# Kernel optimization log

Measured on AMD Instinct MI355X. Metric: run time of the kernel, lower is better.

Reference implementation:

```python
import jax, jax.numpy as jnp
import numpy as np


def _blur(x1, kernel):
    # x1: [B,H,W,1], kernel: [k,k,1,1]; 'same' padding conv, stride 1
    return jax.lax.conv_general_dilated(
        x1, kernel, window_strides=(1, 1), padding='SAME',
        dimension_numbers=('NHWC', 'HWIO', 'NHWC'))


def setup_inputs() -> dict:
    key = jax.random.key(0)
    kx, kk = jax.random.split(key)
    B, H, W, C = 32, 512, 512, 3
    KSZ = 9
    x = jax.random.normal(kx, (B, H, W, C), dtype=jnp.float32)
    # Gaussian-random kernel ~ N(1, 0.05), normalized to sum to 1 (as in normal_kernel)
    kernel = 1.0 + 0.05 * jax.random.normal(kk, (KSZ, KSZ, 1, 1), dtype=jnp.float32)
    kernel = kernel / jnp.sum(kernel)
    return {'x': x, 'kernel': kernel}


def reference(x, kernel):
    # conv2d helper in the original convolves each channel with the SAME kernel
    # then averages across channels; that equals convolving the channel-mean once.
    local_mean = _blur(jnp.mean(x, axis=-1, keepdims=True), kernel)   # [B,H,W,1]
    v = x - local_mean                                                # [B,H,W,C]
    sigma = jnp.sqrt(_blur(jnp.mean(jnp.square(v), axis=-1, keepdims=True), kernel))  # [B,H,W,1]
    mean_sigma = jnp.mean(sigma, axis=(1, 2), keepdims=True)          # [B,1,1,1]
    return v / jnp.maximum(mean_sigma, sigma)
```

## Files before the change

### kernel.cpp

```cpp
#include <hip/hip_runtime.h>

#define BB 32
#define HH 512
#define WW 512
#define HW (HH * WW)
#define NPIX (BB * HH * WW)

#define TILE 64
#define HALO 4
#define RG 72
#define RQ 18
#define NQ (RG * RQ)

__global__ __launch_bounds__(256) void k_moments(const float4* __restrict__ x4,
                                                 float4* __restrict__ m4,
                                                 float4* __restrict__ q4,
                                                 float* __restrict__ sums) {
    int g = blockIdx.x * 256 + threadIdx.x;
    if (blockIdx.x == 0 && threadIdx.x < BB) sums[threadIdx.x] = 0.f;
    if (g >= NPIX / 4) return;
    float4 a = x4[3 * g + 0];
    float4 b = x4[3 * g + 1];
    float4 c = x4[3 * g + 2];
    const float t = 1.f / 3.f;
    float4 m, q;
    m.x = (a.x + a.y + a.z) * t;  q.x = (a.x * a.x + a.y * a.y + a.z * a.z) * t;
    m.y = (a.w + b.x + b.y) * t;  q.y = (a.w * a.w + b.x * b.x + b.y * b.y) * t;
    m.z = (b.z + b.w + c.x) * t;  q.z = (b.z * b.z + b.w * b.w + c.x * c.x) * t;
    m.w = (c.y + c.z + c.w) * t;  q.w = (c.y * c.y + c.z * c.z + c.w * c.w) * t;
    m4[g] = m;
    q4[g] = q;
}

__global__ __launch_bounds__(256) void k_blur_m(const float* __restrict__ src,
                                                const float* __restrict__ kw,
                                                float* __restrict__ dst) {
    __shared__ float tile[RG * RG];
    __shared__ float kk[81];
    const int tx = threadIdx.x, ty = threadIdx.y;
    const int tid = ty * 16 + tx;
    if (tid < 81) kk[tid] = kw[tid];
    const int x0 = blockIdx.x * TILE, y0 = blockIdx.y * TILE;
    const float4* s4 = (const float4*)(src + (size_t)blockIdx.z * HW);
    for (int i = tid; i < NQ; i += 256) {
        int r = i / RQ, q = i - r * RQ;
        int gy = y0 + r - HALO, gx = x0 + 4 * q - HALO;
        float4 v = make_float4(0.f, 0.f, 0.f, 0.f);
        if (gy >= 0 && gy < HH && gx >= 0 && gx < WW) v = s4[(gy * WW + gx) >> 2];
        *(float4*)&tile[r * RG + 4 * q] = v;
    }
    __syncthreads();

    float acc[4][4] = {};
    const float4* t4 = (const float4*)tile;
#pragma unroll
    for (int ky = 0; ky < 9; ++ky) {
        float w[9];
#pragma unroll
        for (int kx = 0; kx < 9; ++kx) w[kx] = kk[ky * 9 + kx];
#pragma unroll
        for (int my = 0; my < 4; ++my) {
            int rr = (4 * ty + my + ky) * RQ + tx;
            float4 a = t4[rr], b = t4[rr + 1], c = t4[rr + 2];
            float f[12] = {a.x, a.y, a.z, a.w, b.x, b.y, b.z, b.w, c.x, c.y, c.z, c.w};
#pragma unroll
            for (int kx = 0; kx < 9; ++kx)
#pragma unroll
                for (int mx = 0; mx < 4; ++mx)
                    acc[my][mx] = fmaf(w[kx], f[mx + kx], acc[my][mx]);
        }
    }
    float* dp = dst + (size_t)blockIdx.z * HW + (size_t)(y0 + 4 * ty) * WW + x0 + 4 * tx;
#pragma unroll
    for (int my = 0; my < 4; ++my)
        *(float4*)(dp + my * WW) = make_float4(acc[my][0], acc[my][1], acc[my][2], acc[my][3]);
}

__global__ __launch_bounds__(256) void k_sigma(const float* __restrict__ m,
                                               const float* __restrict__ q,
                                               const float* __restrict__ lm,
                                               const float* __restrict__ kw,
                                               float* __restrict__ sg,
                                               float* __restrict__ sums) {
    __shared__ float tile[RG * RG];
    __shared__ float kk[81];
    __shared__ float wsum[4];
    const int tx = threadIdx.x, ty = threadIdx.y;
    const int tid = ty * 16 + tx;
    if (tid < 81) kk[tid] = kw[tid];
    const int x0 = blockIdx.x * TILE, y0 = blockIdx.y * TILE;
    const size_t boff = (size_t)blockIdx.z * HW;
    const float4* m4 = (const float4*)(m + boff);
    const float4* q4 = (const float4*)(q + boff);
    const float4* l4 = (const float4*)(lm + boff);
    for (int i = tid; i < NQ; i += 256) {
        int r = i / RQ, qd = i - r * RQ;
        int gy = y0 + r - HALO, gx = x0 + 4 * qd - HALO;
        float4 e = make_float4(0.f, 0.f, 0.f, 0.f);
        if (gy >= 0 && gy < HH && gx >= 0 && gx < WW) {
            int o = (gy * WW + gx) >> 2;
            float4 mm = m4[o], qq = q4[o], ll = l4[o];
            e.x = fmaxf(qq.x - ll.x * (2.f * mm.x - ll.x), 0.f);
            e.y = fmaxf(qq.y - ll.y * (2.f * mm.y - ll.y), 0.f);
            e.z = fmaxf(qq.z - ll.z * (2.f * mm.z - ll.z), 0.f);
            e.w = fmaxf(qq.w - ll.w * (2.f * mm.w - ll.w), 0.f);
        }
        *(float4*)&tile[r * RG + 4 * qd] = e;
    }
    __syncthreads();

    float acc[4][4] = {};
    const float4* t4 = (const float4*)tile;
#pragma unroll
    for (int ky = 0; ky < 9; ++ky) {
        float w[9];
#pragma unroll
        for (int kx = 0; kx < 9; ++kx) w[kx] = kk[ky * 9 + kx];
#pragma unroll
        for (int my = 0; my < 4; ++my) {
            int rr = (4 * ty + my + ky) * RQ + tx;
            float4 a = t4[rr], b = t4[rr + 1], c = t4[rr + 2];
            float f[12] = {a.x, a.y, a.z, a.w, b.x, b.y, b.z, b.w, c.x, c.y, c.z, c.w};
#pragma unroll
            for (int kx = 0; kx < 9; ++kx)
#pragma unroll
                for (int mx = 0; mx < 4; ++mx)
                    acc[my][mx] = fmaf(w[kx], f[mx + kx], acc[my][mx]);
        }
    }
    float s = 0.f;
    float* dp = sg + boff + (size_t)(y0 + 4 * ty) * WW + x0 + 4 * tx;
#pragma unroll
    for (int my = 0; my < 4; ++my) {
        float4 o;
        o.x = sqrtf(fmaxf(acc[my][0], 0.f));
        o.y = sqrtf(fmaxf(acc[my][1], 0.f));
        o.z = sqrtf(fmaxf(acc[my][2], 0.f));
        o.w = sqrtf(fmaxf(acc[my][3], 0.f));
        *(float4*)(dp + my * WW) = o;
        s += o.x + o.y + o.z + o.w;
    }
#pragma unroll
    for (int off = 32; off > 0; off >>= 1) s += __shfl_down(s, off);
    if ((tid & 63) == 0) wsum[tid >> 6] = s;
    __syncthreads();
    if (tid == 0) atomicAdd(&sums[blockIdx.z], wsum[0] + wsum[1] + wsum[2] + wsum[3]);
}

__global__ __launch_bounds__(256) void k_norm(const float4* __restrict__ x4,
                                              const float4* __restrict__ lm4,
                                              const float4* __restrict__ sg4,
                                              const float* __restrict__ sums,
                                              float4* __restrict__ out4) {
    int g = blockIdx.x * 256 + threadIdx.x;
    if (g >= NPIX / 4) return;
    int b = (g * 4) / HW;
    float ms = sums[b] * (1.f / (float)HW);
    float4 l = lm4[g];
    float4 s = sg4[g];
    float i0 = 1.f / fmaxf(ms, s.x);
    float i1 = 1.f / fmaxf(ms, s.y);
    float i2 = 1.f / fmaxf(ms, s.z);
    float i3 = 1.f / fmaxf(ms, s.w);
    float4 a = x4[3 * g + 0];
    float4 bb = x4[3 * g + 1];
    float4 c = x4[3 * g + 2];
    float4 o0, o1, o2;
    o0.x = (a.x - l.x) * i0;  o0.y = (a.y - l.x) * i0;  o0.z = (a.z - l.x) * i0;
    o0.w = (a.w - l.y) * i1;  o1.x = (bb.x - l.y) * i1; o1.y = (bb.y - l.y) * i1;
    o1.z = (bb.z - l.z) * i2; o1.w = (bb.w - l.z) * i2; o2.x = (c.x - l.z) * i2;
    o2.y = (c.y - l.w) * i3;  o2.z = (c.z - l.w) * i3;  o2.w = (c.w - l.w) * i3;
    out4[3 * g + 0] = o0;
    out4[3 * g + 1] = o1;
    out4[3 * g + 2] = o2;
}

extern "C" void kernel_launch(void* const* d_in, const int* in_sizes, int n_in,
                              void* d_out, int out_size, void* d_ws, size_t ws_size,
                              hipStream_t stream) {
    const float* x = (const float*)d_in[0];
    const float* kw = (const float*)d_in[1];
    float* out = (float*)d_out;
    float* wsp = (float*)d_ws;
    float* m    = wsp + 0 * (size_t)NPIX;
    float* q    = wsp + 1 * (size_t)NPIX;
    float* lm   = wsp + 2 * (size_t)NPIX;
    float* sg   = wsp + 3 * (size_t)NPIX;
    float* sums = wsp + 4 * (size_t)NPIX;

    const int ngrp = NPIX / 4;
    k_moments<<<ngrp / 256, 256, 0, stream>>>((const float4*)x, (float4*)m, (float4*)q, sums);

    dim3 blk(16, 16);
    dim3 grd(WW / TILE, HH / TILE, BB);
    k_blur_m<<<grd, blk, 0, stream>>>(m, kw, lm);
    k_sigma<<<grd, blk, 0, stream>>>(m, q, lm, kw, sg, sums);

    k_norm<<<ngrp / 256, 256, 0, stream>>>((const float4*)x, (const float4*)lm,
                                           (const float4*)sg, sums, (float4*)out);
}
```

Measured before the change: 299.1 us.

## Fuse moments, mean blur and sigma blur into one tiled kernel

Merges the channel-moment pass, the local-mean blur and the sigma blur into a single kernel. Each 64x64 tile loads x with an 8-pixel halo, computes mean and square moments in shared memory, and blurs the mean over the 72x72 inner region (recomputing halo work). It then forms the per-pixel variance term in place and blurs it again. This removes the global round trips for m, q and lm between kernels. Per-batch sums are now written as per-block partials and reduced in k_norm, replacing the atomics and the zeroing step. The costs are redundant halo compute, larger shared memory use that may lower occupancy, and filter weights read directly from global memory.

```diff
diff --git a/kernel.cpp b/kernel.cpp
--- a/kernel.cpp
+++ b/kernel.cpp
@@ -7,161 +7,168 @@
 #define NPIX (BB * HH * WW)
 
 #define TILE 64
-#define HALO 4
-#define RG 72
-#define RQ 18
-#define NQ (RG * RQ)
-
-__global__ __launch_bounds__(256) void k_moments(const float4* __restrict__ x4,
-                                                 float4* __restrict__ m4,
-                                                 float4* __restrict__ q4,
-                                                 float* __restrict__ sums) {
-    int g = blockIdx.x * 256 + threadIdx.x;
-    if (blockIdx.x == 0 && threadIdx.x < BB) sums[threadIdx.x] = 0.f;
-    if (g >= NPIX / 4) return;
-    float4 a = x4[3 * g + 0];
-    float4 b = x4[3 * g + 1];
-    float4 c = x4[3 * g + 2];
-    const float t = 1.f / 3.f;
-    float4 m, q;
-    m.x = (a.x + a.y + a.z) * t;  q.x = (a.x * a.x + a.y * a.y + a.z * a.z) * t;
-    m.y = (a.w + b.x + b.y) * t;  q.y = (a.w * a.w + b.x * b.x + b.y * b.y) * t;
-    m.z = (b.z + b.w + c.x) * t;  q.z = (b.z * b.z + b.w * b.w + c.x * c.x) * t;
-    m.w = (c.y + c.z + c.w) * t;  q.w = (c.y * c.y + c.z * c.z + c.w * c.w) * t;
-    m4[g] = m;
-    q4[g] = q;
-}
-
-__global__ __launch_bounds__(256) void k_blur_m(const float* __restrict__ src,
-                                                const float* __restrict__ kw,
-                                                float* __restrict__ dst) {
-    __shared__ float tile[RG * RG];
-    __shared__ float kk[81];
+#define H2 8
+#define RG2 80
+#define RQ2 21
+#define RS2 84
+
+#define LOADROW12(dst, p4, base)                                              \
+    {                                                                         \
+        float4 A_ = (p4)[base], B_ = (p4)[(base) + 1], C_ = (p4)[(base) + 2]; \
+        (dst)[0] = A_.x; (dst)[1] = A_.y; (dst)[2]  = A_.z; (dst)[3]  = A_.w; \
+        (dst)[4] = B_.x; (dst)[5] = B_.y; (dst)[6]  = B_.z; (dst)[7]  = B_.w; \
+        (dst)[8] = C_.x; (dst)[9] = C_.y; (dst)[10] = C_.z; (dst)[11] = C_.w; \
+    }
+
+__global__ __launch_bounds__(256, 3) void k_fused(
+    const float* __restrict__ x, const float* __restrict__ kw,
+    float* __restrict__ lm, float* __restrict__ sg, float* __restrict__ psums)
+{
+    __shared__ float mt[RG2 * RS2];
+    __shared__ float qt[RG2 * RS2];
+    __shared__ float wsum[4];
+
     const int tx = threadIdx.x, ty = threadIdx.y;
     const int tid = ty * 16 + tx;
-    if (tid < 81) kk[tid] = kw[tid];
     const int x0 = blockIdx.x * TILE, y0 = blockIdx.y * TILE;
-    const float4* s4 = (const float4*)(src + (size_t)blockIdx.z * HW);
-    for (int i = tid; i < NQ; i += 256) {
-        int r = i / RQ, q = i - r * RQ;
-        int gy = y0 + r - HALO, gx = x0 + 4 * q - HALO;
-        float4 v = make_float4(0.f, 0.f, 0.f, 0.f);
-        if (gy >= 0 && gy < HH && gx >= 0 && gx < WW) v = s4[(gy * WW + gx) >> 2];
-        *(float4*)&tile[r * RG + 4 * q] = v;
+    const float4* x4 = (const float4*)(x + (size_t)blockIdx.z * HW * 3);
+
+    for (int i = tid; i < RG2 * 20; i += 256) {
+        int r = i / 20, qd = i - r * 20;
+        int gy = y0 + r - H2, gx = x0 + 4 * qd - H2;
+        float4 m = make_float4(0.f, 0.f, 0.f, 0.f);
+        float4 q = make_float4(0.f, 0.f, 0.f, 0.f);
+        if (gy >= 0 && gy < HH && gx >= 0 && gx < WW) {
+            int go = (gy * WW + gx) >> 2;
+            float4 a = x4[3 * go + 0];
+            float4 b = x4[3 * go + 1];
+            float4 c = x4[3 * go + 2];
+            const float t = 1.f / 3.f;
+            m.x = (a.x + a.y + a.z) * t;  q.x = (a.x * a.x + a.y * a.y + a.z * a.z) * t;
+            m.y = (a.w + b.x + b.y) * t;  q.y = (a.w * a.w + b.x * b.x + b.y * b.y) * t;
+            m.z = (b.z + b.w + c.x) * t;  q.z = (b.z * b.z + b.w * b.w + c.x * c.x) * t;
+            m.w = (c.y + c.z + c.w) * t;  q.w = (c.y * c.y + c.z * c.z + c.w * c.w) * t;
+        }
+        *(float4*)&mt[r * RS2 + 4 * qd] = m;
+        *(float4*)&qt[r * RS2 + 4 * qd] = q;
     }
     __syncthreads();
 
-    float acc[4][4] = {};
-    const float4* t4 = (const float4*)tile;
-#pragma unroll
-    for (int ky = 0; ky < 9; ++ky) {
-        float w[9];
-#pragma unroll
-        for (int kx = 0; kx < 9; ++kx) w[kx] = kk[ky * 9 + kx];
+    const float4* m4t = (const float4*)mt;
+    float* lmg = lm + (size_t)blockIdx.z * HW;
+
+#pragma unroll 1
+    for (int t = tid; t < 324; t += 256) {
+        int tr = t / 18;
+        int q0 = t - tr * 18;
+        int r0 = tr * 4;
+        float fw[4][12];
+#pragma unroll
+        for (int j = 0; j < 3; ++j) LOADROW12(fw[j], m4t, (r0 + j) * RQ2 + q0);
+        float acc[4][4] = {};
+#pragma unroll
+        for (int ky = 0; ky < 9; ++ky) {
+            LOADROW12(fw[(ky + 3) & 3], m4t, (r0 + ky + 3) * RQ2 + q0);
+            float w[9];
+#pragma unroll
+            for (int kx = 0; kx < 9; ++kx) w[kx] = kw[ky * 9 + kx];
+#pragma unroll
+            for (int my = 0; my < 4; ++my)
+#pragma unroll
+                for (int kx = 0; kx < 9; ++kx)
+#pragma unroll
+                    for (int mx = 0; mx < 4; ++mx)
+                        acc[my][mx] = fmaf(w[kx], fw[(my + ky) & 3][mx + kx], acc[my][mx]);
+        }
+        const int gxb = x0 + 4 * q0 - 4;
+        const bool xin = (gxb >= 0) && (gxb < WW);
+        const bool wr = (r0 >= 4) && (r0 < 68) && (q0 >= 1) && (q0 < 17);
+#pragma unroll
+        for (int row = 0; row < 4; ++row) {
+            int gy = y0 + r0 + row - 4;
+            float4 l = make_float4(acc[row][0], acc[row][1], acc[row][2], acc[row][3]);
+            int off = (r0 + row + 4) * RS2 + 4 * q0 + 4;
+            float4 mm = *(const float4*)&mt[off];
+            float4* qp = (float4*)&qt[off];
+            float4 qq = *qp;
+            float4 e = make_float4(0.f, 0.f, 0.f, 0.f);
+            if (xin && gy >= 0 && gy < HH) {
+                e.x = fmaxf(qq.x - l.x * (2.f * mm.x - l.x), 0.f);
+                e.y = fmaxf(qq.y - l.y * (2.f * mm.y - l.y), 0.f);
+                e.z = fmaxf(qq.z - l.z * (2.f * mm.z - l.z), 0.f);
+                e.w = fmaxf(qq.w - l.w * (2.f * mm.w - l.w), 0.f);
+            }
+            *qp = e;
+            if (wr) *(float4*)(lmg + (size_t)gy * WW + gxb) = l;
+        }
+    }
+    __syncthreads();
+
+    {
+        const float4* q4t = (const float4*)qt;
+        const int cb = tx + 1;
+        float fw[4][12];
+#pragma unroll
+        for (int j = 0; j < 3; ++j) LOADROW12(fw[j], q4t, (4 * ty + j + 4) * RQ2 + cb);
+        float acc[4][4] = {};
+#pragma unroll
+        for (int ky = 0; ky < 9; ++ky) {
+            LOADROW12(fw[(ky + 3) & 3], q4t, (4 * ty + ky + 7) * RQ2 + cb);
+            float w[9];
+#pragma unroll
+            for (int kx = 0; kx < 9; ++kx) w[kx] = kw[ky * 9 + kx];
+#pragma unroll
+            for (int my = 0; my < 4; ++my)
+#pragma unroll
+                for (int kx = 0; kx < 9; ++kx)
+#pragma unroll
+                    for (int mx = 0; mx < 4; ++mx)
+                        acc[my][mx] = fmaf(w[kx], fw[(my + ky) & 3][mx + kx], acc[my][mx]);
+        }
+        float s = 0.f;
+        float* dp = sg + (size_t)blockIdx.z * HW + (size_t)(y0 + 4 * ty) * WW + x0 + 4 * tx;
 #pragma unroll
         for (int my = 0; my < 4; ++my) {
-            int rr = (4 * ty + my + ky) * RQ + tx;
-            float4 a = t4[rr], b = t4[rr + 1], c = t4[rr + 2];
-            float f[12] = {a.x, a.y, a.z, a.w, b.x, b.y, b.z, b.w, c.x, c.y, c.z, c.w};
-#pragma unroll
-            for (int kx = 0; kx < 9; ++kx)
-#pragma unroll
-                for (int mx = 0; mx < 4; ++mx)
-                    acc[my][mx] = fmaf(w[kx], f[mx + kx], acc[my][mx]);
-        }
-    }
-    float* dp = dst + (size_t)blockIdx.z * HW + (size_t)(y0 + 4 * ty) * WW + x0 + 4 * tx;
-#pragma unroll
-    for (int my = 0; my < 4; ++my)
-        *(float4*)(dp + my * WW) = make_float4(acc[my][0], acc[my][1], acc[my][2], acc[my][3]);
-}
-
-__global__ __launch_bounds__(256) void k_sigma(const float* __restrict__ m,
-                                               const float* __restrict__ q,
-                                               const float* __restrict__ lm,
-                                               const float* __restrict__ kw,
-                                               float* __restrict__ sg,
-                                               float* __restrict__ sums) {
-    __shared__ float tile[RG * RG];
-    __shared__ float kk[81];
-    __shared__ float wsum[4];
-    const int tx = threadIdx.x, ty = threadIdx.y;
-    const int tid = ty * 16 + tx;
-    if (tid < 81) kk[tid] = kw[tid];
-    const int x0 = blockIdx.x * TILE, y0 = blockIdx.y * TILE;
-    const size_t boff = (size_t)blockIdx.z * HW;
-    const float4* m4 = (const float4*)(m + boff);
-    const float4* q4 = (const float4*)(q + boff);
-    const float4* l4 = (const float4*)(lm + boff);
-    for (int i = tid; i < NQ; i += 256) {
-        int r = i / RQ, qd = i - r * RQ;
-        int gy = y0 + r - HALO, gx = x0 + 4 * qd - HALO;
-        float4 e = make_float4(0.f, 0.f, 0.f, 0.f);
-        if (gy >= 0 && gy < HH && gx >= 0 && gx < WW) {
-            int o = (gy * WW + gx) >> 2;
-            float4 mm = m4[o], qq = q4[o], ll = l4[o];
-            e.x = fmaxf(qq.x - ll.x * (2.f * mm.x - ll.x), 0.f);
-            e.y = fmaxf(qq.y - ll.y * (2.f * mm.y - ll.y), 0.f);
-            e.z = fmaxf(qq.z - ll.z * (2.f * mm.z - ll.z), 0.f);
-            e.w = fmaxf(qq.w - ll.w * (2.f * mm.w - ll.w), 0.f);
-        }
-        *(float4*)&tile[r * RG + 4 * qd] = e;
-    }
-    __syncthreads();
-
-    float acc[4][4] = {};
-    const float4* t4 = (const float4*)tile;
-#pragma unroll
-    for (int ky = 0; ky < 9; ++ky) {
-        float w[9];
-#pragma unroll
-        for (int kx = 0; kx < 9; ++kx) w[kx] = kk[ky * 9 + kx];
-#pragma unroll
-        for (int my = 0; my < 4; ++my) {
-            int rr = (4 * ty + my + ky) * RQ + tx;
-            float4 a = t4[rr], b = t4[rr + 1], c = t4[rr + 2];
-            float f[12] = {a.x, a.y, a.z, a.w, b.x, b.y, b.z, b.w, c.x, c.y, c.z, c.w};
-#pragma unroll
-            for (int kx = 0; kx < 9; ++kx)
-#pragma unroll
-                for (int mx = 0; mx < 4; ++mx)
-                    acc[my][mx] = fmaf(w[kx], f[mx + kx], acc[my][mx]);
-        }
-    }
-    float s = 0.f;
-    float* dp = sg + boff + (size_t)(y0 + 4 * ty) * WW + x0 + 4 * tx;
-#pragma unroll
-    for (int my = 0; my < 4; ++my) {
-        float4 o;
-        o.x = sqrtf(fmaxf(acc[my][0], 0.f));
-        o.y = sqrtf(fmaxf(acc[my][1], 0.f));
-        o.z = sqrtf(fmaxf(acc[my][2], 0.f));
-        o.w = sqrtf(fmaxf(acc[my][3], 0.f));
-        *(float4*)(dp + my * WW) = o;
-        s += o.x + o.y + o.z + o.w;
-    }
-#pragma unroll
-    for (int off = 32; off > 0; off >>= 1) s += __shfl_down(s, off);
-    if ((tid & 63) == 0) wsum[tid >> 6] = s;
-    __syncthreads();
-    if (tid == 0) atomicAdd(&sums[blockIdx.z], wsum[0] + wsum[1] + wsum[2] + wsum[3]);
+            float4 o;
+            o.x = sqrtf(fmaxf(acc[my][0], 0.f));
+            o.y = sqrtf(fmaxf(acc[my][1], 0.f));
+            o.z = sqrtf(fmaxf(acc[my][2], 0.f));
+            o.w = sqrtf(fmaxf(acc[my][3], 0.f));
+            *(float4*)(dp + my * WW) = o;
+            s += o.x + o.y + o.z + o.w;
+        }
+#pragma unroll
+        for (int off = 32; off > 0; off >>= 1) s += __shfl_down(s, off);
+        if ((tid & 63) == 0) wsum[tid >> 6] = s;
+        __syncthreads();
+        if (tid == 0)
+            psums[blockIdx.z * 64 + blockIdx.y * 8 + blockIdx.x] =
+                wsum[0] + wsum[1] + wsum[2] + wsum[3];
+    }
 }
 
 __global__ __launch_bounds__(256) void k_norm(const float4* __restrict__ x4,
                                               const float4* __restrict__ lm4,
                                               const float4* __restrict__ sg4,
-                                              const float* __restrict__ sums,
+                                              const float* __restrict__ psums,
                                               float4* __restrict__ out4) {
+    __shared__ float msh;
     int g = blockIdx.x * 256 + threadIdx.x;
-    if (g >= NPIX / 4) return;
-    int b = (g * 4) / HW;
-    float ms = sums[b] * (1.f / (float)HW);
+    int b = g >> 16;
+    float s = 0.f;
+    if (threadIdx.x < 64) s = psums[b * 64 + threadIdx.x];
+#pragma unroll
+    for (int off = 32; off > 0; off >>= 1) s += __shfl_down(s, off);
+    if (threadIdx.x == 0) msh = s * (1.f / (float)HW);
+    __syncthreads();
+    float ms = msh;
+
     float4 l = lm4[g];
-    float4 s = sg4[g];
-    float i0 = 1.f / fmaxf(ms, s.x);
-    float i1 = 1.f / fmaxf(ms, s.y);
-    float i2 = 1.f / fmaxf(ms, s.z);
-    float i3 = 1.f / fmaxf(ms, s.w);
+    float4 sv = sg4[g];
+    float i0 = 1.f / fmaxf(ms, sv.x);
+    float i1 = 1.f / fmaxf(ms, sv.y);
+    float i2 = 1.f / fmaxf(ms, sv.z);
+    float i3 = 1.f / fmaxf(ms, sv.w);
     float4 a = x4[3 * g + 0];
     float4 bb = x4[3 * g + 1];
     float4 c = x4[3 * g + 2];
@@ -182,20 +189,14 @@
     const float* kw = (const float*)d_in[1];
     float* out = (float*)d_out;
     float* wsp = (float*)d_ws;
-    float* m    = wsp + 0 * (size_t)NPIX;
-    float* q    = wsp + 1 * (size_t)NPIX;
-    float* lm   = wsp + 2 * (size_t)NPIX;
-    float* sg   = wsp + 3 * (size_t)NPIX;
-    float* sums = wsp + 4 * (size_t)NPIX;
-
-    const int ngrp = NPIX / 4;
-    k_moments<<<ngrp / 256, 256, 0, stream>>>((const float4*)x, (float4*)m, (float4*)q, sums);
+    float* lmb = wsp;
+    float* sgb = wsp + (size_t)NPIX;
+    float* ps  = wsp + 2 * (size_t)NPIX;
 
     dim3 blk(16, 16);
     dim3 grd(WW / TILE, HH / TILE, BB);
-    k_blur_m<<<grd, blk, 0, stream>>>(m, kw, lm);
-    k_sigma<<<grd, blk, 0, stream>>>(m, q, lm, kw, sg, sums);
-
-    k_norm<<<ngrp / 256, 256, 0, stream>>>((const float4*)x, (const float4*)lm,
-                                           (const float4*)sg, sums, (float4*)out);
+    k_fused<<<grd, blk, 0, stream>>>(x, kw, lmb, sgb, ps);
+
+    k_norm<<<NPIX / 4 / 256, 256, 0, stream>>>((const float4*)x, (const float4*)lmb,
+                                               (const float4*)sgb, ps, (float4*)out);
 }
```

Measured after the change: 391.0 us. 30.7% more time.
